# Kernel optimization log

Hardware: AMD Instinct MI355X
Metric: run time of the kernel (lower is better)

The kernel has to match this reference:

```python
import jax, jax.numpy as jnp
import numpy as np

N, E, IN, K, F, D = 50000, 800000, 256, 4, 64, 2


def setup_inputs() -> dict:
    key = jax.random.key(0)
    ks = jax.random.split(key, 10)
    # CSR rowptr: 0 .. E, nondecreasing, endpoints pinned
    inner = jnp.sort(jax.random.randint(ks[0], (N - 1,), 0, E + 1))
    rowptr = jnp.concatenate([jnp.zeros(1, jnp.int64), inner.astype(jnp.int64), jnp.full(1, E, jnp.int64)])
    colind = jax.random.randint(ks[1], (E,), 0, N).astype(jnp.int64)
    # CSC mirrors (used only by the fused kernel's backward; inert in forward math)
    inner_c = jnp.sort(jax.random.randint(ks[2], (N - 1,), 0, E + 1))
    colptr = jnp.concatenate([jnp.zeros(1, jnp.int64), inner_c.astype(jnp.int64), jnp.full(1, E, jnp.int64)])
    rowind = jax.random.randint(ks[3], (E,), 0, N).astype(jnp.int64)
    permute = jnp.arange(E, dtype=jnp.int64)
    feat = jax.random.normal(ks[4], (N, IN), dtype=jnp.float32)
    pseudo = jax.random.uniform(ks[5], (E, D), dtype=jnp.float32)
    # params: fc weight [K*F, IN] (xavier-normal style scale), mu ~ N(0, 0.1), inv_sigma = 1, bias = 0
    gain = float(np.sqrt(2.0))
    std = gain * float(np.sqrt(2.0 / (IN + K * F)))
    W_fc = jax.random.normal(ks[6], (K * F, IN), dtype=jnp.float32) * std
    mu = jax.random.normal(ks[7], (K, D), dtype=jnp.float32) * 0.1
    inv_sigma = jnp.ones((K, D), dtype=jnp.float32)
    bias = jnp.zeros((F,), dtype=jnp.float32)
    return {"rowptr": rowptr, "colind": colind, "colptr": colptr, "rowind": rowind,
            "permute": permute, "feat": feat, "pseudo": pseudo,
            "W_fc": W_fc, "mu": mu, "inv_sigma": inv_sigma, "bias": bias}


def reference(rowptr, colind, colptr, rowind, permute, feat, pseudo, W_fc, mu, inv_sigma, bias):
    n = feat.shape[0]
    e = colind.shape[0]
    k, d = mu.shape
    f = W_fc.shape[0] // k
    # dense projection: [N, K, F]
    node_feat = (feat @ W_fc.T).reshape(n, k, f)
    # per-edge Gaussian mixture weights: [E, K]
    diff = pseudo[:, None, :] - mu[None, :, :]              # [E, K, D]
    gaussian = jnp.exp(jnp.sum(-0.5 * diff * diff * (inv_sigma[None, :, :] ** 2), axis=-1))
    # multi-head SpMM: gather source feats, weight per kernel, sum kernels (sum commutes
    # with the segment reduction, so fold the head-sum into the edge message): [E, F]
    msg = jnp.einsum('ek,ekf->ef', gaussian, node_feat[colind])
    # destination node of each CSR edge
    dst = jnp.searchsorted(rowptr, jnp.arange(e), side='right') - 1
    rst = jax.ops.segment_sum(msg, dst, num_segments=n)      # [N, F]
    return rst + bias
```

## Files before the change

kernel.cpp:

```cpp
#include <hip/hip_runtime.h>


typedef _Float16 f16;
typedef __attribute__((ext_vector_type(4))) _Float16 f16x4;
typedef __attribute__((ext_vector_type(8))) _Float16 f16x8;
typedef __attribute__((ext_vector_type(4))) float f32x4;

__device__ inline f16x4 cvt4h(float4 v) {
    f16x4 h;
    h.x = (f16)v.x; h.y = (f16)v.y; h.z = (f16)v.z; h.w = (f16)v.w;
    return h;
}

__device__ inline int dot4_i8(int a, int b) {
#if __has_builtin(__builtin_amdgcn_sdot4)
    return __builtin_amdgcn_sdot4(a, b, 0, false);
#else
    return (int)(char)(a)       * (int)(char)(b)
         + (int)(char)(a >> 8)  * (int)(char)(b >> 8)
         + (int)(char)(a >> 16) * (int)(char)(b >> 16)
         + (int)(char)(a >> 24) * (int)(char)(b >> 24);
#endif
}

__global__ __launch_bounds__(256) void convert_W(
    const float* __restrict__ W, f16* __restrict__ Wp)
{
    const int gid = blockIdx.x * 256 + threadIdx.x;
    const int jp = gid >> 6, k4 = gid & 63;
    const int wrow = ((jp & 3) << 6) | (jp >> 2);
    reinterpret_cast<f16x4*>(Wp)[jp * 64 + k4] =
        cvt4h(reinterpret_cast<const float4*>(W)[wrow * 64 + k4]);
}

#define ASTRIDE 264
#define AS_BYTES (64 * ASTRIDE * 2)

__global__ __launch_bounds__(256) void gemm_fused(
    const float* __restrict__ feat,
    const f16* __restrict__ Wp,
    char* __restrict__ nfq,
    float* __restrict__ sc,
    int M)
{
    __shared__ char smem[AS_BYTES + 256 * 32 * 2];
    f16* As = (f16*)smem;
    f16* Bs = (f16*)(smem + AS_BYTES);
    char* qt = smem + AS_BYTES;
    const int t    = threadIdx.x;
    const int lane = t & 63;
    const int wave = t >> 6;
    const int bm   = blockIdx.x * 64;
    const int l16  = lane & 15;
    const int quad = lane >> 4;
    const int wn   = wave * 64;

    size_t bsrc[4];
#pragma unroll
    for (int j = 0; j < 4; ++j)
        bsrc[j] = (size_t)(wave * 64 + j * 16 + (lane >> 2)) * 256 + (lane & 3) * 8;

    typedef __attribute__((address_space(3))) void lds_t;
    typedef const __attribute__((address_space(1))) void gm_t;

#pragma unroll
    for (int j = 0; j < 4; ++j)
        __builtin_amdgcn_global_load_lds((gm_t*)(Wp + bsrc[j]),
            (lds_t*)(Bs + (wave * 4 + j) * 512), 16, 0, 0);

#pragma unroll
    for (int it = 0; it < 8; ++it) {
        const int flat = it * 2048 + t * 8;
        const int row  = flat >> 8;
        const int koff = flat & 255;
        const float* src = feat + (size_t)min(bm + row, M - 1) * 256 + koff;
        const float4 a0 = *reinterpret_cast<const float4*>(src);
        const float4 a1 = *reinterpret_cast<const float4*>(src + 4);
        *reinterpret_cast<f16x4*>(&As[row * ASTRIDE + koff])     = cvt4h(a0);
        *reinterpret_cast<f16x4*>(&As[row * ASTRIDE + koff + 4]) = cvt4h(a1);
    }

    f32x4 acc[4][4];
#pragma unroll
    for (int mi = 0; mi < 4; ++mi)
#pragma unroll
        for (int ni = 0; ni < 4; ++ni)
            acc[mi][ni] = (f32x4){0.f, 0.f, 0.f, 0.f};

    for (int ki = 0; ki < 8; ++ki) {
        __syncthreads();

        f16x8 af[4], bfr[4];
#pragma unroll
        for (int mi = 0; mi < 4; ++mi)
            af[mi] = *reinterpret_cast<const f16x8*>(
                &As[(mi * 16 + l16) * ASTRIDE + ki * 32 + quad * 8]);
#pragma unroll
        for (int ni = 0; ni < 4; ++ni)
            bfr[ni] = *reinterpret_cast<const f16x8*>(
                &Bs[(wn + ni * 16 + l16) * 32 + quad * 8]);

        __syncthreads();
        if (ki < 7) {
            const int k0 = (ki + 1) * 32;
#pragma unroll
            for (int j = 0; j < 4; ++j)
                __builtin_amdgcn_global_load_lds((gm_t*)(Wp + bsrc[j] + k0),
                    (lds_t*)(Bs + (wave * 4 + j) * 512), 16, 0, 0);
        }
#pragma unroll
        for (int mi = 0; mi < 4; ++mi)
#pragma unroll
            for (int ni = 0; ni < 4; ++ni)
                acc[mi][ni] = __builtin_amdgcn_mfma_f32_16x16x32_f16(
                    af[mi], bfr[ni], acc[mi][ni], 0, 0, 0);
    }

#pragma unroll
    for (int mi = 0; mi < 4; ++mi) {
#pragma unroll
        for (int r = 0; r < 4; ++r) {
            float am = 0.f;
#pragma unroll
            for (int ni = 0; ni < 4; ++ni)
                am = fmaxf(am, fabsf(acc[mi][ni][r]));
            am = fmaxf(am, __shfl_xor(am, 1));
            am = fmaxf(am, __shfl_xor(am, 2));
            am = fmaxf(am, __shfl_xor(am, 4));
            am = fmaxf(am, __shfl_xor(am, 8));
            const float sinv = am > 0.f ? 127.f / am : 0.f;
            const int rl = mi * 16 + quad * 4 + r;
#pragma unroll
            for (int ni = 0; ni < 4; ++ni)
                qt[rl * 256 + wn + ni * 16 + l16] =
                    (char)(int)__builtin_rintf(acc[mi][ni][r] * sinv);
            if (l16 == 0) {
                const int row = bm + rl;
                if (row < M) sc[row * 4 + wave] = am * (1.f / 16129.f);
            }
        }
    }
    __syncthreads();

    {
        const int rl  = t >> 2;
        const int co  = (t & 3) * 64;
        const int row = bm + rl;
        if (row < M) {
            const int4* s4 = reinterpret_cast<const int4*>(qt + rl * 256 + co);
            int4* d4 = reinterpret_cast<int4*>(nfq + (size_t)row * 256 + co);
#pragma unroll
            for (int j = 0; j < 4; ++j) d4[j] = s4[j];
        }
    }
}

__global__ __launch_bounds__(128) void edge_aggregate(
    const int* __restrict__ rowptr,
    const int* __restrict__ colind,
    const float* __restrict__ pseudo,
    const char* __restrict__ nfq,
    const float* __restrict__ sc,
    const float* __restrict__ mu,
    const float* __restrict__ inv_sigma,
    const float* __restrict__ bias,
    float* __restrict__ out,
    int N)
{
    __shared__ int gpack[2][16];
    __shared__ int cbuf[2][16];
    const int wave = threadIdx.x >> 6;
    const int lane = threadIdx.x & 63;
    const int node = blockIdx.x * 2 + wave;
    if (node >= N) return;

    const int kk = lane >> 4;
    const int ii = lane & 15;
    const float mx = mu[2 * kk], my = mu[2 * kk + 1];
    const float sa = inv_sigma[2 * kk], sb = inv_sigma[2 * kk + 1];
    const float sx = sa * sa, sy = sb * sb;

    const int e0 = rowptr[node];
    const int e1 = rowptr[node + 1];
    int* gp = gpack[wave];
    int* cw = cbuf[wave];

    float a4[4] = {0.f, 0.f, 0.f, 0.f};
    for (int ec = e0; ec < e1; ec += 16) {
        const int cnt = min(16, e1 - ec);
        {
            const bool v = ii < cnt;
            const int e = v ? (ec + ii) : e0;
            const float2 p = *reinterpret_cast<const float2*>(pseudo + 2 * (size_t)e);
            const float dx = p.x - mx, dy = p.y - my;
            const float g = v ? __expf(-0.5f * (dx * dx * sx + dy * dy * sy)) : 0.f;
            ((char*)&gp[ii])[kk] = (char)(int)(g * 127.f + 0.5f);
            if (kk == 0) cw[ii] = v ? colind[e] : 0;
        }
        __builtin_amdgcn_wave_barrier();
        __threadfence_block();
        const int cnt4 = (cnt + 3) & ~3;
        for (int i2 = 0; i2 < cnt4; i2 += 4) {
#pragma unroll
            for (int j = 0; j < 4; ++j) {
                const int c = cw[i2 + j];
                const int q = *reinterpret_cast<const int*>(
                    nfq + ((size_t)c << 8) + (lane << 2));
                const float s = sc[c * 4 + (lane >> 4)];
                const int d = dot4_i8(q, gp[i2 + j]);
                a4[j] += s * (float)d;
            }
        }
        __builtin_amdgcn_wave_barrier();
        __threadfence_block();
    }
    out[((size_t)node << 6) + lane] =
        (a4[0] + a4[1]) + (a4[2] + a4[3]) + bias[lane];
}

extern "C" void kernel_launch(void* const* d_in, const int* in_sizes, int n_in,
                              void* d_out, int out_size, void* d_ws, size_t ws_size,
                              hipStream_t stream)
{
    const int*   rowptr    = (const int*)d_in[0];
    const int*   colind    = (const int*)d_in[1];
    const float* feat      = (const float*)d_in[5];
    const float* pseudo    = (const float*)d_in[6];
    const float* W_fc      = (const float*)d_in[7];
    const float* mu        = (const float*)d_in[8];
    const float* inv_sigma = (const float*)d_in[9];
    const float* bias      = (const float*)d_in[10];
    float* out = (float*)d_out;

    const int N = in_sizes[0] - 1;
    char*  nfq = (char*)d_ws;
    float* sc  = (float*)(nfq + (size_t)N * 256);
    f16*   Wp  = (f16*)d_out;

    hipLaunchKernelGGL(convert_W, dim3(64), dim3(256), 0, stream, W_fc, Wp);

    hipLaunchKernelGGL(gemm_fused, dim3((N + 63) / 64), dim3(256), 0, stream,
                       feat, Wp, nfq, sc, N);

    hipLaunchKernelGGL(edge_aggregate, dim3((N + 1) / 2), dim3(128), 0, stream,
                       rowptr, colind, pseudo, nfq, sc, mu, inv_sigma, bias, out, N);
}
```

Measured before the change: 187.8 us.

## Restructure edge aggregation to split 4 edge groups per wave with 16-byte gathers

Each wave now splits its 64 lanes into 4 edge groups of 16 lanes. Each lane gathers a 16-byte int4 slice of a neighbour's quantized row instead of a 4-byte int, and the partial sums are reduced across groups with shuffles at the end. Gaussian weights are computed once per edge with all four kernels in one lane using exp2f, then passed around by shuffle. This removes the LDS staging and wave barriers. The aim is fewer, wider memory transactions and more gathers in flight, at the cost of a cross-lane reduction and extra registers.

```diff
diff --git a/kernel.cpp b/kernel.cpp
--- a/kernel.cpp
+++ b/kernel.cpp
@@ -167,55 +167,81 @@
     float* __restrict__ out,
     int N)
 {
-    __shared__ int gpack[2][16];
-    __shared__ int cbuf[2][16];
     const int wave = threadIdx.x >> 6;
     const int lane = threadIdx.x & 63;
     const int node = blockIdx.x * 2 + wave;
     if (node >= N) return;
 
-    const int kk = lane >> 4;
-    const int ii = lane & 15;
-    const float mx = mu[2 * kk], my = mu[2 * kk + 1];
-    const float sa = inv_sigma[2 * kk], sb = inv_sigma[2 * kk + 1];
-    const float sx = sa * sa, sy = sb * sb;
+    const int fo = lane & 15;
+    const int eg = lane >> 4;
+    const int qoff = fo << 4;
+    const int goff = fo >> 2;
+
+    float mxk[4], myk[4], cxk[4], cyk[4];
+#pragma unroll
+    for (int k = 0; k < 4; ++k) {
+        mxk[k] = mu[2 * k];
+        myk[k] = mu[2 * k + 1];
+        const float a = inv_sigma[2 * k], b = inv_sigma[2 * k + 1];
+        const float c = -0.5f * 1.4426950408889634f;
+        cxk[k] = c * a * a;
+        cyk[k] = c * b * b;
+    }
 
     const int e0 = rowptr[node];
     const int e1 = rowptr[node + 1];
-    int* gp = gpack[wave];
-    int* cw = cbuf[wave];
-
-    float a4[4] = {0.f, 0.f, 0.f, 0.f};
+
+    float acc0 = 0.f, acc1 = 0.f, acc2 = 0.f, acc3 = 0.f;
+
     for (int ec = e0; ec < e1; ec += 16) {
-        const int cnt = min(16, e1 - ec);
-        {
-            const bool v = ii < cnt;
-            const int e = v ? (ec + ii) : e0;
-            const float2 p = *reinterpret_cast<const float2*>(pseudo + 2 * (size_t)e);
-            const float dx = p.x - mx, dy = p.y - my;
-            const float g = v ? __expf(-0.5f * (dx * dx * sx + dy * dy * sy)) : 0.f;
-            ((char*)&gp[ii])[kk] = (char)(int)(g * 127.f + 0.5f);
-            if (kk == 0) cw[ii] = v ? colind[e] : 0;
-        }
-        __builtin_amdgcn_wave_barrier();
-        __threadfence_block();
-        const int cnt4 = (cnt + 3) & ~3;
-        for (int i2 = 0; i2 < cnt4; i2 += 4) {
-#pragma unroll
-            for (int j = 0; j < 4; ++j) {
-                const int c = cw[i2 + j];
-                const int q = *reinterpret_cast<const int*>(
-                    nfq + ((size_t)c << 8) + (lane << 2));
-                const float s = sc[c * 4 + (lane >> 4)];
-                const int d = dot4_i8(q, gp[i2 + j]);
-                a4[j] += s * (float)d;
-            }
-        }
-        __builtin_amdgcn_wave_barrier();
-        __threadfence_block();
-    }
-    out[((size_t)node << 6) + lane] =
-        (a4[0] + a4[1]) + (a4[2] + a4[3]) + bias[lane];
+        const int exm = ec + fo;
+        const bool gv = exm < e1;
+        const int ex  = gv ? exm : e1 - 1;
+        const float2 p = *reinterpret_cast<const float2*>(pseudo + 2 * (size_t)ex);
+        int gpk = 0;
+#pragma unroll
+        for (int k = 0; k < 4; ++k) {
+            const float dx = p.x - mxk[k], dy = p.y - myk[k];
+            const float g = exp2f(dx * dx * cxk[k] + dy * dy * cyk[k]);
+            gpk |= ((int)(g * 127.f + 0.5f)) << (8 * k);
+        }
+        if (!gv) gpk = 0;
+
+        int4  q[4];
+        float s[4];
+        int   gq[4];
+#pragma unroll
+        for (int gi = 0; gi < 4; ++gi) {
+            const int ei = min(ec + gi * 4 + eg, e1 - 1);
+            const int c  = colind[ei];
+            q[gi]  = *reinterpret_cast<const int4*>(
+                         nfq + ((size_t)c << 8) + qoff);
+            s[gi]  = sc[c * 4 + goff];
+            gq[gi] = __shfl(gpk, gi * 4 + eg);
+        }
+#pragma unroll
+        for (int gi = 0; gi < 4; ++gi) {
+            acc0 = fmaf(s[gi], (float)dot4_i8(q[gi].x, gq[gi]), acc0);
+            acc1 = fmaf(s[gi], (float)dot4_i8(q[gi].y, gq[gi]), acc1);
+            acc2 = fmaf(s[gi], (float)dot4_i8(q[gi].z, gq[gi]), acc2);
+            acc3 = fmaf(s[gi], (float)dot4_i8(q[gi].w, gq[gi]), acc3);
+        }
+    }
+
+    acc0 += __shfl_xor(acc0, 16); acc0 += __shfl_xor(acc0, 32);
+    acc1 += __shfl_xor(acc1, 16); acc1 += __shfl_xor(acc1, 32);
+    acc2 += __shfl_xor(acc2, 16); acc2 += __shfl_xor(acc2, 32);
+    acc3 += __shfl_xor(acc3, 16); acc3 += __shfl_xor(acc3, 32);
+
+    if (lane < 16) {
+        const float4 b4 = reinterpret_cast<const float4*>(bias)[fo];
+        float4 o;
+        o.x = acc0 + b4.x;
+        o.y = acc1 + b4.y;
+        o.z = acc2 + b4.z;
+        o.w = acc3 + b4.w;
+        reinterpret_cast<float4*>(out + ((size_t)node << 6))[fo] = o;
+    }
 }
 
 extern "C" void kernel_launch(void* const* d_in, const int* in_sizes, int n_in,
```

After: 166.8 us. 1.13x faster.
